# Optimization experiments

Hardware: AMD Instinct MI355X
Metric: run time of the kernel (lower is better)

## Reference

```python
import jax, jax.numpy as jnp
import numpy as np

G, N, F, H, B, L = 4, 1024, 256, 256, 32, 4


def setup_inputs() -> dict:
    key = jax.random.key(0)
    ks = jax.random.split(key, 8)
    batch_xs = jax.random.normal(ks[0], (G, N, F), dtype=jnp.float32)
    # dense (preprocessed/normalized) adjacency; scale ~1/N keeps activations stable
    batch_as = jax.random.uniform(ks[1], (G, N, N), dtype=jnp.float32) / N
    w_in = jax.random.normal(ks[2], (F, H), dtype=jnp.float32) * 0.05
    b_in = jnp.zeros((H,), dtype=jnp.float32)
    gcn_w = jax.random.normal(ks[3], (L, H, H), dtype=jnp.float32) * 0.05
    gcn_b = jnp.zeros((L, H), dtype=jnp.float32)
    graph_idx = jax.random.randint(ks[4], (B,), 0, G)
    cp_mask = jax.random.randint(ks[5], (B, N), 0, 2).astype(bool)
    return {"batch_xs": batch_xs, "batch_as": batch_as, "w_in": w_in, "b_in": b_in,
            "gcn_w": gcn_w, "gcn_b": gcn_b, "graph_idx": graph_idx, "cp_mask": cp_mask}


def reference(batch_xs, batch_as, w_in, b_in, gcn_w, gcn_b, graph_idx, cp_mask):
    # gather_nd: select per-example graph features and adjacency
    X = batch_xs[graph_idx]          # [B, N, F]
    A = batch_as[graph_idx]          # [B, N, N]
    # GNN input dense layer (relu); dropout is identity at inference
    x = jax.nn.relu(X @ w_in + b_in)  # [B, N, H]
    res = x                           # residual from post-input activations
    # GCNConv stack: act(A @ x @ W + b); relu for all but final tanh layer
    for i in range(L - 1):
        x = jax.nn.relu(jnp.einsum('bnm,bmh->bnh', A, x) @ gcn_w[i] + gcn_b[i])
    x = jnp.tanh(jnp.einsum('bnm,bmh->bnh', A, x) @ gcn_w[L - 1] + gcn_b[L - 1])
    x = x + res
    # ragged boolean_mask + reduce_mean over nodes == masked mean
    m = cp_mask.astype(x.dtype)       # [B, N]
    denom = jnp.maximum(jnp.sum(m, axis=1, keepdims=True), 1.0)
    return jnp.sum(x * m[..., None], axis=1) / denom  # [B, H]
```

## Files before the change

### kernel.cpp

```cpp
#include <hip/hip_runtime.h>
#include <math.h>

#define G 4
#define NN 1024
#define FF 256
#define HH 256
#define BB 32
#define LL 4

typedef __attribute__((ext_vector_type(8))) short short8;
typedef __attribute__((ext_vector_type(8))) unsigned short ushort8;
typedef __attribute__((ext_vector_type(4))) unsigned short ushort4v;
typedef __attribute__((ext_vector_type(4))) float floatx4;

__device__ inline unsigned short f2bf(float f) {
  union { float f; unsigned u; } x; x.f = f;
  unsigned r = x.u + 0x7fffu + ((x.u >> 16) & 1u);
  return (unsigned short)(r >> 16);
}
__device__ inline float bf2f(unsigned short u) {
  union { unsigned u; float f; } x; x.u = (unsigned)u << 16;
  return x.f;
}

__device__ void in_tile(int job, const float* __restrict__ X,
                        const float* __restrict__ w_in,
                        const float* __restrict__ b_in,
                        unsigned short* __restrict__ xbf,
                        unsigned short* __restrict__ h0bf, unsigned short* As,
                        unsigned short* Bs, int t) {
  const int nt_ = job & 3, mt = (job >> 2) & 15, g = job >> 6;
  const int m0 = mt * 64, n0 = nt_ * 64;
  const int lane = t & 63, w = t >> 6;
  const int wm = w & 1, wn = w >> 1;
  const int l16 = lane & 15, quad = lane >> 4;

  floatx4 acc[2][2];
#pragma unroll
  for (int i = 0; i < 2; ++i)
#pragma unroll
    for (int j = 0; j < 2; ++j) acc[i][j] = (floatx4){0.f, 0.f, 0.f, 0.f};

  for (int tt = 0; tt < 4; ++tt) {
    const int kb = tt * 64;
    __syncthreads();
#pragma unroll
    for (int i = 0; i < 2; ++i) {
      const int q = t + i * 256;
      const int row = q >> 3, c8 = q & 7;
      const float* Af =
          X + (long)g * NN * FF + (long)(m0 + row) * FF + kb + c8 * 8;
      float4 f0 = *(const float4*)Af;
      float4 f1 = *(const float4*)(Af + 4);
      ushort8 v;
      v[0] = f2bf(f0.x); v[1] = f2bf(f0.y); v[2] = f2bf(f0.z); v[3] = f2bf(f0.w);
      v[4] = f2bf(f1.x); v[5] = f2bf(f1.y); v[6] = f2bf(f1.z); v[7] = f2bf(f1.w);
      *(ushort8*)&As[row * 72 + c8 * 8] = v;
    }
    {
      const int row = t >> 2;
      const int c0 = (t & 3) * 16;
#pragma unroll
      for (int j = 0; j < 4; ++j) {
        float4 f = *(const float4*)&w_in[(long)(kb + row) * HH + n0 + c0 + j * 4];
        Bs[(c0 + j * 4 + 0) * 72 + row] = f2bf(f.x);
        Bs[(c0 + j * 4 + 1) * 72 + row] = f2bf(f.y);
        Bs[(c0 + j * 4 + 2) * 72 + row] = f2bf(f.z);
        Bs[(c0 + j * 4 + 3) * 72 + row] = f2bf(f.w);
      }
    }
    __syncthreads();
#pragma unroll
    for (int kk = 0; kk < 64; kk += 32) {
      const int ko = kk + quad * 8;
      short8 a0 = *(const short8*)&As[(wm * 32 + l16) * 72 + ko];
      short8 a1 = *(const short8*)&As[(wm * 32 + 16 + l16) * 72 + ko];
      short8 b0 = *(const short8*)&Bs[(wn * 32 + l16) * 72 + ko];
      short8 b1 = *(const short8*)&Bs[(wn * 32 + 16 + l16) * 72 + ko];
      acc[0][0] = __builtin_amdgcn_mfma_f32_16x16x32_bf16(a0, b0, acc[0][0], 0, 0, 0);
      acc[0][1] = __builtin_amdgcn_mfma_f32_16x16x32_bf16(a0, b1, acc[0][1], 0, 0, 0);
      acc[1][0] = __builtin_amdgcn_mfma_f32_16x16x32_bf16(a1, b0, acc[1][0], 0, 0, 0);
      acc[1][1] = __builtin_amdgcn_mfma_f32_16x16x32_bf16(a1, b1, acc[1][1], 0, 0, 0);
    }
  }

#pragma unroll
  for (int i = 0; i < 2; ++i) {
#pragma unroll
    for (int j = 0; j < 2; ++j) {
      const int n = n0 + wn * 32 + j * 16 + l16;
      const int mB = m0 + wm * 32 + i * 16 + quad * 4;
      const float bv = b_in[n];
#pragma unroll
      for (int r = 0; r < 4; ++r) {
        const unsigned short pv = f2bf(fmaxf(acc[i][j][r] + bv, 0.f));
        xbf[(long)g * NN * HH + (long)(mB + r) * HH + n] = pv;
        h0bf[(long)g * NN * HH + (long)(mB + r) * HH + n] = pv;
      }
    }
  }
}

__device__ void mask_job(int b, const void* __restrict__ cp_mask,
                         float* __restrict__ fmask, float* __restrict__ denom,
                         int t) {
  const unsigned char* bytes = (const unsigned char*)cp_mask;
  __shared__ int fmt;
  __shared__ float red[256];
  if (t == 0) {
    int any = 0;
    for (int i = 0; i < 256; ++i)
      if ((i & 3) && bytes[i]) any = 1;
    fmt = any ? 0 : 1;
  }
  __syncthreads();
  float cnt = 0.f;
  for (int n = t; n < NN; n += 256) {
    float v;
    if (fmt)
      v = ((const int*)cp_mask)[b * NN + n] ? 1.f : 0.f;
    else
      v = bytes[b * NN + n] ? 1.f : 0.f;
    fmask[b * NN + n] = v;
    cnt += v;
  }
  red[t] = cnt;
  __syncthreads();
  for (int s = 128; s > 0; s >>= 1) {
    if (t < s) red[t] += red[t + s];
    __syncthreads();
  }
  if (t == 0) denom[b] = fmaxf(red[0], 1.f);
}

__device__ void gw_job(int j, const float* __restrict__ gcn_w,
                       unsigned short* __restrict__ gwT, int t) {
  const int l = j >> 4, r0 = (j & 15) * 16;
  const float* src = gcn_w + (long)l * HH * HH;
  unsigned short* dst = gwT + (long)l * HH * HH;
  unsigned short vv[16];
#pragma unroll
  for (int rr = 0; rr < 16; ++rr) vv[rr] = f2bf(src[(long)(r0 + rr) * HH + t]);
  *(ushort8*)&dst[(long)t * HH + r0] = *(ushort8*)&vv[0];
  *(ushort8*)&dst[(long)t * HH + r0 + 8] = *(ushort8*)&vv[8];
}

__global__ __launch_bounds__(256) void pre_kernel(
    const float* __restrict__ batch_as, unsigned short* __restrict__ Abf,
    const float* __restrict__ batch_xs, const float* __restrict__ w_in,
    const float* __restrict__ b_in, unsigned short* __restrict__ xbf,
    unsigned short* __restrict__ h0bf, const float* __restrict__ gcn_w,
    unsigned short* __restrict__ gwT, const void* __restrict__ cp_mask,
    float* __restrict__ fmask, float* __restrict__ denom,
    float* __restrict__ out) {
  __shared__ __align__(16) unsigned short As[64 * 72];
  __shared__ __align__(16) unsigned short Bs[64 * 72];
  const int b = blockIdx.x, t = threadIdx.x;
  if (b < 1024) {
    const long idx = ((long)b * 256 + t) * 16;
#pragma unroll
    for (int h = 0; h < 2; ++h) {
      float4 f0 = *(const float4*)&batch_as[idx + h * 8];
      float4 f1 = *(const float4*)&batch_as[idx + h * 8 + 4];
      ushort8 v;
      v[0] = f2bf(f0.x); v[1] = f2bf(f0.y); v[2] = f2bf(f0.z); v[3] = f2bf(f0.w);
      v[4] = f2bf(f1.x); v[5] = f2bf(f1.y); v[6] = f2bf(f1.z); v[7] = f2bf(f1.w);
      *(ushort8*)&Abf[idx + h * 8] = v;
    }
  } else if (b < 1280) {
    in_tile(b - 1024, batch_xs, w_in, b_in, xbf, h0bf, As, Bs, t);
  } else if (b < 1344) {
    gw_job(b - 1280, gcn_w, gwT, t);
  } else if (b < 1376) {
    mask_job(b - 1344, cp_mask, fmask, denom, t);
  } else {
    for (int i = 0; i < 32; ++i) out[i * 256 + t] = 0.f;
  }
}

__global__ __launch_bounds__(256) void g1_kernel(
    const unsigned short* __restrict__ xbf,
    const unsigned short* __restrict__ WT,
    unsigned short* __restrict__ yT) {
  __shared__ __align__(16) unsigned short As[64 * 72];
  __shared__ __align__(16) unsigned short Bs[64 * 72];
  const int n0 = blockIdx.x * 64;
  const int m0 = blockIdx.y * 64;
  const int g = blockIdx.z;
  const int t = threadIdx.x;
  const int lane = t & 63, w = t >> 6;
  const int wm = w & 1, wn = w >> 1;
  const int l16 = lane & 15, quad = lane >> 4;

  const unsigned short* Ab = xbf + (long)g * NN * HH;

  ushort8 pa[2], pb[2];
  auto load_tile = [&](int tt) {
    const int kb = tt * 64;
#pragma unroll
    for (int i = 0; i < 2; ++i) {
      const int q = t + i * 256;
      const int row = q >> 3, c8 = q & 7;
      pa[i] = *(const ushort8*)&Ab[(long)(m0 + row) * HH + kb + c8 * 8];
      pb[i] = *(const ushort8*)&WT[(long)(n0 + row) * HH + kb + c8 * 8];
    }
  };
  auto store_tile = [&]() {
#pragma unroll
    for (int i = 0; i < 2; ++i) {
      const int q = t + i * 256;
      const int row = q >> 3, c8 = q & 7;
      *(ushort8*)&As[row * 72 + c8 * 8] = pa[i];
      *(ushort8*)&Bs[row * 72 + c8 * 8] = pb[i];
    }
  };

  floatx4 acc[2][2];
#pragma unroll
  for (int i = 0; i < 2; ++i)
#pragma unroll
    for (int j = 0; j < 2; ++j) acc[i][j] = (floatx4){0.f, 0.f, 0.f, 0.f};

  load_tile(0);
  for (int tt = 0; tt < 4; ++tt) {
    __syncthreads();
    store_tile();
    __syncthreads();
    if (tt + 1 < 4) load_tile(tt + 1);
#pragma unroll
    for (int kk = 0; kk < 64; kk += 32) {
      const int ko = kk + quad * 8;
      short8 a0 = *(const short8*)&As[(wm * 32 + l16) * 72 + ko];
      short8 a1 = *(const short8*)&As[(wm * 32 + 16 + l16) * 72 + ko];
      short8 b0 = *(const short8*)&Bs[(wn * 32 + l16) * 72 + ko];
      short8 b1 = *(const short8*)&Bs[(wn * 32 + 16 + l16) * 72 + ko];
      acc[0][0] = __builtin_amdgcn_mfma_f32_16x16x32_bf16(a0, b0, acc[0][0], 0, 0, 0);
      acc[0][1] = __builtin_amdgcn_mfma_f32_16x16x32_bf16(a0, b1, acc[0][1], 0, 0, 0);
      acc[1][0] = __builtin_amdgcn_mfma_f32_16x16x32_bf16(a1, b0, acc[1][0], 0, 0, 0);
      acc[1][1] = __builtin_amdgcn_mfma_f32_16x16x32_bf16(a1, b1, acc[1][1], 0, 0, 0);
    }
  }

#pragma unroll
  for (int i = 0; i < 2; ++i) {
#pragma unroll
    for (int j = 0; j < 2; ++j) {
      const int n = n0 + wn * 32 + j * 16 + l16;
      const int mB = m0 + wm * 32 + i * 16 + quad * 4;
      ushort4v pv;
#pragma unroll
      for (int r = 0; r < 4; ++r) pv[r] = f2bf(acc[i][j][r]);
      *(ushort4v*)&yT[(long)g * HH * NN + (long)n * NN + mB] = pv;
    }
  }
}

template <int ACT>
__global__ __launch_bounds__(256) void g2_kernel(
    const unsigned short* __restrict__ Abf,
    const unsigned short* __restrict__ yT, const float* __restrict__ bias,
    const unsigned short* __restrict__ h0bf, unsigned short* __restrict__ xbf,
    const float* __restrict__ fmask, const float* __restrict__ denom,
    const int* __restrict__ gidx, float* __restrict__ out) {
  __shared__ __align__(16) unsigned short As[32 * 136];
  __shared__ __align__(16) unsigned short Bs[64 * 136];
  const int n0 = blockIdx.x * 64;
  const int m0 = blockIdx.y * 32;
  const int g = blockIdx.z;
  const int t = threadIdx.x;
  const int lane = t & 63, w = t >> 6;
  const int wm = w & 1, wn = w >> 1;
  const int l16 = lane & 15, quad = lane >> 4;

  const unsigned short* Ag = Abf + (long)g * NN * NN + (long)m0 * NN;
  const unsigned short* Bg = yT + (long)g * HH * NN + (long)n0 * NN;

  ushort8 pa[2], pb[4];
  auto load_tile = [&](int tt) {
    const int kb = tt * 128;
#pragma unroll
    for (int i = 0; i < 2; ++i) {
      const int q = t + i * 256;
      const int row = q >> 4, c8 = q & 15;
      pa[i] = *(const ushort8*)&Ag[(long)row * NN + kb + c8 * 8];
    }
#pragma unroll
    for (int i = 0; i < 4; ++i) {
      const int q = t + i * 256;
      const int row = q >> 4, c8 = q & 15;
      pb[i] = *(const ushort8*)&Bg[(long)row * NN + kb + c8 * 8];
    }
  };
  auto store_tile = [&]() {
#pragma unroll
    for (int i = 0; i < 2; ++i) {
      const int q = t + i * 256;
      const int row = q >> 4, c8 = q & 15;
      *(ushort8*)&As[row * 136 + c8 * 8] = pa[i];
    }
#pragma unroll
    for (int i = 0; i < 4; ++i) {
      const int q = t + i * 256;
      const int row = q >> 4, c8 = q & 15;
      *(ushort8*)&Bs[row * 136 + c8 * 8] = pb[i];
    }
  };

  floatx4 acc[2];
  acc[0] = (floatx4){0.f, 0.f, 0.f, 0.f};
  acc[1] = (floatx4){0.f, 0.f, 0.f, 0.f};

  load_tile(0);
  for (int tt = 0; tt < 8; ++tt) {
    __syncthreads();
    store_tile();
    __syncthreads();
    if (tt + 1 < 8) load_tile(tt + 1);
#pragma unroll
    for (int kk = 0; kk < 128; kk += 32) {
      const int ko = kk + quad * 8;
      short8 a = *(const short8*)&As[(wm * 16 + l16) * 136 + ko];
      short8 b0 = *(const short8*)&Bs[(wn * 32 + l16) * 136 + ko];
      short8 b1 = *(const short8*)&Bs[(wn * 32 + 16 + l16) * 136 + ko];
      acc[0] = __builtin_amdgcn_mfma_f32_16x16x32_bf16(a, b0, acc[0], 0, 0, 0);
      acc[1] = __builtin_amdgcn_mfma_f32_16x16x32_bf16(a, b1, acc[1], 0, 0, 0);
    }
  }

  if (ACT == 1) {
#pragma unroll
    for (int j = 0; j < 2; ++j) {
      const int n = n0 + wn * 32 + j * 16 + l16;
      const int mB = m0 + wm * 16 + quad * 4;
      const float bv = bias[n];
#pragma unroll
      for (int r = 0; r < 4; ++r)
        xbf[(long)g * NN * HH + (long)(mB + r) * HH + n] =
            f2bf(fmaxf(acc[j][r] + bv, 0.f));
    }
  } else {
    const int mB0 = m0 + wm * 16 + quad * 4;
    float zv[2][4];
#pragma unroll
    for (int j = 0; j < 2; ++j) {
      const int n = n0 + wn * 32 + j * 16 + l16;
      const float bv = bias[n];
#pragma unroll
      for (int r = 0; r < 4; ++r) {
        const long idx = (long)g * NN * HH + (long)(mB0 + r) * HH + n;
        zv[j][r] = tanhf(acc[j][r] + bv) + bf2f(h0bf[idx]);
      }
    }
    for (int b = 0; b < BB; ++b) {
      if (gidx[b] != g) continue;
      const float invd = 1.f / denom[b];
      float m4[4];
#pragma unroll
      for (int r = 0; r < 4; ++r) m4[r] = fmask[b * NN + mB0 + r];
#pragma unroll
      for (int j = 0; j < 2; ++j) {
        float p = m4[0] * zv[j][0] + m4[1] * zv[j][1] + m4[2] * zv[j][2] +
                  m4[3] * zv[j][3];
        p += __shfl_xor(p, 16);
        p += __shfl_xor(p, 32);
        if (quad == 0) {
          const int n = n0 + wn * 32 + j * 16 + l16;
          atomicAdd(&out[b * HH + n], p * invd);
        }
      }
    }
  }
}

extern "C" void kernel_launch(void* const* d_in, const int* in_sizes, int n_in,
                              void* d_out, int out_size, void* d_ws,
                              size_t ws_size, hipStream_t stream) {
  (void)in_sizes; (void)n_in; (void)out_size; (void)ws_size;
  const float* batch_xs = (const float*)d_in[0];
  const float* batch_as = (const float*)d_in[1];
  const float* w_in = (const float*)d_in[2];
  const float* b_in = (const float*)d_in[3];
  const float* gcn_w = (const float*)d_in[4];
  const float* gcn_b = (const float*)d_in[5];
  const int* graph_idx = (const int*)d_in[6];
  const void* cp_mask = d_in[7];
  float* out = (float*)d_out;

  char* p = (char*)d_ws;
  unsigned short* Abf = (unsigned short*)p;  p += (long)G * NN * NN * 2;
  unsigned short* gwT = (unsigned short*)p;  p += (long)LL * HH * HH * 2;
  unsigned short* xbf = (unsigned short*)p;  p += (long)G * NN * HH * 2;
  unsigned short* h0bf = (unsigned short*)p; p += (long)G * NN * HH * 2;
  unsigned short* yT = (unsigned short*)p;   p += (long)G * HH * NN * 2;
  float* fmask = (float*)p;                  p += (long)BB * NN * 4;
  float* denom = (float*)p;                  p += BB * 4;

  pre_kernel<<<1377, 256, 0, stream>>>(batch_as, Abf, batch_xs, w_in, b_in,
                                       xbf, h0bf, gcn_w, gwT, cp_mask, fmask,
                                       denom, out);

  for (int l = 0; l < LL; ++l) {
    g1_kernel<<<dim3(4, 16, G), 256, 0, stream>>>(
        xbf, gwT + (long)l * HH * HH, yT);
    if (l < LL - 1)
      g2_kernel<1><<<dim3(4, 32, G), 256, 0, stream>>>(
          Abf, yT, gcn_b + (long)l * HH, nullptr, xbf, nullptr, nullptr,
          nullptr, nullptr);
    else
      g2_kernel<0><<<dim3(4, 32, G), 256, 0, stream>>>(
          Abf, yT, gcn_b + (long)l * HH, h0bf, nullptr, fmask, denom,
          graph_idx, out);
  }
}
```

Measured before the change: 147.1 us.

## Fuse adjacency matmul with next layer's weight matmul per row block

Adds a fused kernel that computes relu(A@y + b) for a 16-row block and immediately multiplies it by the next layer's weight matrix, writing the transposed result directly. This replaces the separate g1/g2 launch pairs for the middle layers, removing the intermediate xbf round-trip and three kernel launches. In exchange the grid is much smaller (256 blocks of 512 threads) with a large shared-memory footprint, and each block re-reads the full transposed y for its graph, which may lower occupancy and parallelism.

```diff
diff --git a/kernel.cpp b/kernel.cpp
--- a/kernel.cpp
+++ b/kernel.cpp
@@ -252,6 +252,127 @@
       for (int r = 0; r < 4; ++r) pv[r] = f2bf(acc[i][j][r]);
       *(ushort4v*)&yT[(long)g * HH * NN + (long)n * NN + mB] = pv;
     }
+  }
+}
+
+__global__ __launch_bounds__(512) void fused_kernel(
+    const unsigned short* __restrict__ Abf,
+    const unsigned short* __restrict__ yT, const float* __restrict__ bias,
+    const unsigned short* __restrict__ WT, unsigned short* __restrict__ y2T) {
+  __shared__ __align__(16) unsigned short As[16 * 136];
+  __shared__ __align__(16) unsigned short Bs[256 * 136];
+  __shared__ __align__(16) unsigned short Xs[16 * 264];
+  const int m0 = blockIdx.x * 16;
+  const int g = blockIdx.y;
+  const int t = threadIdx.x;
+  const int lane = t & 63, w = t >> 6;
+  const int l16 = lane & 15, quad = lane >> 4;
+
+  const unsigned short* Ag = Abf + (long)g * NN * NN + (long)m0 * NN;
+  const unsigned short* Bg = yT + (long)g * HH * NN;
+
+  ushort8 pb[8], pa;
+  auto load_tile = [&](int tt) {
+    const int kb = tt * 128;
+#pragma unroll
+    for (int i = 0; i < 8; ++i) {
+      const int q = t + i * 512;
+      const int row = q >> 4, c8 = q & 15;
+      pb[i] = *(const ushort8*)&Bg[(long)row * NN + kb + c8 * 8];
+    }
+    if (t < 256) {
+      const int row = t >> 4, c8 = t & 15;
+      pa = *(const ushort8*)&Ag[(long)row * NN + kb + c8 * 8];
+    }
+  };
+  auto store_tile = [&]() {
+#pragma unroll
+    for (int i = 0; i < 8; ++i) {
+      const int q = t + i * 512;
+      const int row = q >> 4, c8 = q & 15;
+      *(ushort8*)&Bs[row * 136 + c8 * 8] = pb[i];
+    }
+    if (t < 256) {
+      const int row = t >> 4, c8 = t & 15;
+      *(ushort8*)&As[row * 136 + c8 * 8] = pa;
+    }
+  };
+
+  floatx4 acc[2];
+  acc[0] = (floatx4){0.f, 0.f, 0.f, 0.f};
+  acc[1] = (floatx4){0.f, 0.f, 0.f, 0.f};
+
+  load_tile(0);
+  for (int tt = 0; tt < 8; ++tt) {
+    __syncthreads();
+    store_tile();
+    __syncthreads();
+    if (tt + 1 < 8) load_tile(tt + 1);
+#pragma unroll
+    for (int kk = 0; kk < 128; kk += 32) {
+      const int ko = kk + quad * 8;
+      short8 a = *(const short8*)&As[l16 * 136 + ko];
+      short8 b0 = *(const short8*)&Bs[(w * 32 + l16) * 136 + ko];
+      short8 b1 = *(const short8*)&Bs[(w * 32 + 16 + l16) * 136 + ko];
+      acc[0] = __builtin_amdgcn_mfma_f32_16x16x32_bf16(a, b0, acc[0], 0, 0, 0);
+      acc[1] = __builtin_amdgcn_mfma_f32_16x16x32_bf16(a, b1, acc[1], 0, 0, 0);
+    }
+  }
+
+  ushort8 pw[8];
+  auto loadW = [&](int t2) {
+    const int kb = t2 * 128;
+#pragma unroll
+    for (int i = 0; i < 8; ++i) {
+      const int q = t + i * 512;
+      const int row = q >> 4, c8 = q & 15;
+      pw[i] = *(const ushort8*)&WT[(long)row * HH + kb + c8 * 8];
+    }
+  };
+  loadW(0);
+
+#pragma unroll
+  for (int j = 0; j < 2; ++j) {
+    const int n = w * 32 + j * 16 + l16;
+    const float bv = bias[n];
+#pragma unroll
+    for (int r = 0; r < 4; ++r)
+      Xs[(quad * 4 + r) * 264 + n] = f2bf(fmaxf(acc[j][r] + bv, 0.f));
+  }
+
+  floatx4 acc2[2];
+  acc2[0] = (floatx4){0.f, 0.f, 0.f, 0.f};
+  acc2[1] = (floatx4){0.f, 0.f, 0.f, 0.f};
+
+  for (int t2 = 0; t2 < 2; ++t2) {
+    __syncthreads();
+#pragma unroll
+    for (int i = 0; i < 8; ++i) {
+      const int q = t + i * 512;
+      const int row = q >> 4, c8 = q & 15;
+      *(ushort8*)&Bs[row * 136 + c8 * 8] = pw[i];
+    }
+    __syncthreads();
+    if (t2 == 0) loadW(1);
+    const int kb = t2 * 128;
+#pragma unroll
+    for (int kk = 0; kk < 128; kk += 32) {
+      const int ko = kk + quad * 8;
+      short8 a = *(const short8*)&Xs[l16 * 264 + kb + ko];
+      short8 b0 = *(const short8*)&Bs[(w * 32 + l16) * 136 + ko];
+      short8 b1 = *(const short8*)&Bs[(w * 32 + 16 + l16) * 136 + ko];
+      acc2[0] = __builtin_amdgcn_mfma_f32_16x16x32_bf16(a, b0, acc2[0], 0, 0, 0);
+      acc2[1] = __builtin_amdgcn_mfma_f32_16x16x32_bf16(a, b1, acc2[1], 0, 0, 0);
+    }
+  }
+
+#pragma unroll
+  for (int j = 0; j < 2; ++j) {
+    const int n = w * 32 + j * 16 + l16;
+    ushort4v pv;
+#pragma unroll
+    for (int r = 0; r < 4; ++r) pv[r] = f2bf(acc2[j][r]);
+    *(ushort4v*)&y2T[(long)g * HH * NN + (long)n * NN + m0 + quad * 4] = pv;
   }
 }
 
@@ -391,7 +512,8 @@
   unsigned short* gwT = (unsigned short*)p;  p += (long)LL * HH * HH * 2;
   unsigned short* xbf = (unsigned short*)p;  p += (long)G * NN * HH * 2;
   unsigned short* h0bf = (unsigned short*)p; p += (long)G * NN * HH * 2;
-  unsigned short* yT = (unsigned short*)p;   p += (long)G * HH * NN * 2;
+  unsigned short* yTa = (unsigned short*)p;  p += (long)G * HH * NN * 2;
+  unsigned short* yTb = (unsigned short*)p;  p += (long)G * HH * NN * 2;
   float* fmask = (float*)p;                  p += (long)BB * NN * 4;
   float* denom = (float*)p;                  p += BB * 4;
 
@@ -399,16 +521,16 @@
                                        xbf, h0bf, gcn_w, gwT, cp_mask, fmask,
                                        denom, out);
 
-  for (int l = 0; l < LL; ++l) {
-    g1_kernel<<<dim3(4, 16, G), 256, 0, stream>>>(
-        xbf, gwT + (long)l * HH * HH, yT);
-    if (l < LL - 1)
-      g2_kernel<1><<<dim3(4, 32, G), 256, 0, stream>>>(
-          Abf, yT, gcn_b + (long)l * HH, nullptr, xbf, nullptr, nullptr,
-          nullptr, nullptr);
-    else
-      g2_kernel<0><<<dim3(4, 32, G), 256, 0, stream>>>(
-          Abf, yT, gcn_b + (long)l * HH, h0bf, nullptr, fmask, denom,
-          graph_idx, out);
-  }
-}
+  g1_kernel<<<dim3(4, 16, G), 256, 0, stream>>>(xbf, gwT, yTa);
+
+  fused_kernel<<<dim3(64, G), 512, 0, stream>>>(
+      Abf, yTa, gcn_b + 0 * HH, gwT + (long)1 * HH * HH, yTb);
+  fused_kernel<<<dim3(64, G), 512, 0, stream>>>(
+      Abf, yTb, gcn_b + 1 * HH, gwT + (long)2 * HH * HH, yTa);
+  fused_kernel<<<dim3(64, G), 512, 0, stream>>>(
+      Abf, yTa, gcn_b + 2 * HH, gwT + (long)3 * HH * HH, yTb);
+
+  g2_kernel<0><<<dim3(4, 32, G), 256, 0, stream>>>(
+      Abf, yTb, gcn_b + (long)3 * HH, h0bf, nullptr, fmask, denom,
+      graph_idx, out);
+}
```

Measured after the change: 149.5 us. About the same (+1.7%).

## Fuse input layer with first GCN weight matmul in pre-kernel

Applied to the files above, without the earlier changes.

The pre-kernel's input dense-layer tiles now compute full 64x256 row blocks and chain straight into the layer-0 weight matmul, writing the transposed product directly. This removes the first g1_kernel launch and the xbf round trip for layer 0, and ping-pongs between two yT buffers. The cost is far fewer, heavier tiles (64 blocks instead of 256) that use much more shared memory and registers, and the output zeroing is folded into the mask blocks.

```diff
diff --git a/kernel.cpp b/kernel.cpp
--- a/kernel.cpp
+++ b/kernel.cpp
@@ -23,23 +23,21 @@
   return x.f;
 }
 
-__device__ void in_tile(int job, const float* __restrict__ X,
-                        const float* __restrict__ w_in,
-                        const float* __restrict__ b_in,
-                        unsigned short* __restrict__ xbf,
-                        unsigned short* __restrict__ h0bf, unsigned short* As,
-                        unsigned short* Bs, int t) {
-  const int nt_ = job & 3, mt = (job >> 2) & 15, g = job >> 6;
-  const int m0 = mt * 64, n0 = nt_ * 64;
+__device__ void in64_tile(int job, const float* __restrict__ X,
+                          const float* __restrict__ w_in,
+                          const float* __restrict__ b_in,
+                          const float* __restrict__ gcn_w0,
+                          unsigned short* __restrict__ h0bf,
+                          unsigned short* __restrict__ yT, unsigned short* As,
+                          unsigned short* Bs, unsigned short* Xs, int t) {
+  const int mt = job & 15, g = job >> 4;
+  const int m0 = mt * 64;
   const int lane = t & 63, w = t >> 6;
-  const int wm = w & 1, wn = w >> 1;
   const int l16 = lane & 15, quad = lane >> 4;
 
-  floatx4 acc[2][2];
-#pragma unroll
-  for (int i = 0; i < 2; ++i)
-#pragma unroll
-    for (int j = 0; j < 2; ++j) acc[i][j] = (floatx4){0.f, 0.f, 0.f, 0.f};
+  floatx4 acc[16];
+#pragma unroll
+  for (int j = 0; j < 16; ++j) acc[j] = (floatx4){0.f, 0.f, 0.f, 0.f};
 
   for (int tt = 0; tt < 4; ++tt) {
     const int kb = tt * 64;
@@ -61,43 +59,88 @@
       const int row = t >> 2;
       const int c0 = (t & 3) * 16;
 #pragma unroll
-      for (int j = 0; j < 4; ++j) {
-        float4 f = *(const float4*)&w_in[(long)(kb + row) * HH + n0 + c0 + j * 4];
-        Bs[(c0 + j * 4 + 0) * 72 + row] = f2bf(f.x);
-        Bs[(c0 + j * 4 + 1) * 72 + row] = f2bf(f.y);
-        Bs[(c0 + j * 4 + 2) * 72 + row] = f2bf(f.z);
-        Bs[(c0 + j * 4 + 3) * 72 + row] = f2bf(f.w);
+      for (int nb = 0; nb < 4; ++nb) {
+#pragma unroll
+        for (int jj = 0; jj < 4; ++jj) {
+          float4 f = *(const float4*)&w_in[(long)(kb + row) * HH + nb * 64 +
+                                           c0 + jj * 4];
+          Bs[(nb * 64 + c0 + jj * 4 + 0) * 72 + row] = f2bf(f.x);
+          Bs[(nb * 64 + c0 + jj * 4 + 1) * 72 + row] = f2bf(f.y);
+          Bs[(nb * 64 + c0 + jj * 4 + 2) * 72 + row] = f2bf(f.z);
+          Bs[(nb * 64 + c0 + jj * 4 + 3) * 72 + row] = f2bf(f.w);
+        }
       }
     }
     __syncthreads();
 #pragma unroll
     for (int kk = 0; kk < 64; kk += 32) {
       const int ko = kk + quad * 8;
-      short8 a0 = *(const short8*)&As[(wm * 32 + l16) * 72 + ko];
-      short8 a1 = *(const short8*)&As[(wm * 32 + 16 + l16) * 72 + ko];
-      short8 b0 = *(const short8*)&Bs[(wn * 32 + l16) * 72 + ko];
-      short8 b1 = *(const short8*)&Bs[(wn * 32 + 16 + l16) * 72 + ko];
-      acc[0][0] = __builtin_amdgcn_mfma_f32_16x16x32_bf16(a0, b0, acc[0][0], 0, 0, 0);
-      acc[0][1] = __builtin_amdgcn_mfma_f32_16x16x32_bf16(a0, b1, acc[0][1], 0, 0, 0);
-      acc[1][0] = __builtin_amdgcn_mfma_f32_16x16x32_bf16(a1, b0, acc[1][0], 0, 0, 0);
-      acc[1][1] = __builtin_amdgcn_mfma_f32_16x16x32_bf16(a1, b1, acc[1][1], 0, 0, 0);
-    }
-  }
-
-#pragma unroll
-  for (int i = 0; i < 2; ++i) {
-#pragma unroll
-    for (int j = 0; j < 2; ++j) {
-      const int n = n0 + wn * 32 + j * 16 + l16;
-      const int mB = m0 + wm * 32 + i * 16 + quad * 4;
-      const float bv = b_in[n];
-#pragma unroll
-      for (int r = 0; r < 4; ++r) {
-        const unsigned short pv = f2bf(fmaxf(acc[i][j][r] + bv, 0.f));
-        xbf[(long)g * NN * HH + (long)(mB + r) * HH + n] = pv;
-        h0bf[(long)g * NN * HH + (long)(mB + r) * HH + n] = pv;
-      }
-    }
+      short8 a = *(const short8*)&As[(w * 16 + l16) * 72 + ko];
+#pragma unroll
+      for (int j = 0; j < 16; ++j) {
+        short8 b = *(const short8*)&Bs[(j * 16 + l16) * 72 + ko];
+        acc[j] = __builtin_amdgcn_mfma_f32_16x16x32_bf16(a, b, acc[j], 0, 0, 0);
+      }
+    }
+  }
+
+#pragma unroll
+  for (int j = 0; j < 16; ++j) {
+    const int n = j * 16 + l16;
+    const float bv = b_in[n];
+#pragma unroll
+    for (int r = 0; r < 4; ++r) {
+      const int mr = w * 16 + quad * 4 + r;
+      const unsigned short pv = f2bf(fmaxf(acc[j][r] + bv, 0.f));
+      h0bf[(long)g * NN * HH + (long)(m0 + mr) * HH + n] = pv;
+      Xs[mr * 264 + n] = pv;
+    }
+  }
+
+  floatx4 acc2[16];
+#pragma unroll
+  for (int j = 0; j < 16; ++j) acc2[j] = (floatx4){0.f, 0.f, 0.f, 0.f};
+
+  for (int tt = 0; tt < 4; ++tt) {
+    const int kb = tt * 64;
+    __syncthreads();
+    {
+      const int row = t >> 2;
+      const int c0 = (t & 3) * 16;
+#pragma unroll
+      for (int nb = 0; nb < 4; ++nb) {
+#pragma unroll
+        for (int jj = 0; jj < 4; ++jj) {
+          float4 f = *(const float4*)&gcn_w0[(long)(kb + row) * HH + nb * 64 +
+                                             c0 + jj * 4];
+          Bs[(nb * 64 + c0 + jj * 4 + 0) * 72 + row] = f2bf(f.x);
+          Bs[(nb * 64 + c0 + jj * 4 + 1) * 72 + row] = f2bf(f.y);
+          Bs[(nb * 64 + c0 + jj * 4 + 2) * 72 + row] = f2bf(f.z);
+          Bs[(nb * 64 + c0 + jj * 4 + 3) * 72 + row] = f2bf(f.w);
+        }
+      }
+    }
+    __syncthreads();
+#pragma unroll
+    for (int kk = 0; kk < 64; kk += 32) {
+      const int ko = kk + quad * 8;
+      short8 a = *(const short8*)&Xs[(w * 16 + l16) * 264 + kb + ko];
+#pragma unroll
+      for (int j = 0; j < 16; ++j) {
+        short8 b = *(const short8*)&Bs[(j * 16 + l16) * 72 + ko];
+        acc2[j] = __builtin_amdgcn_mfma_f32_16x16x32_bf16(a, b, acc2[j], 0, 0, 0);
+      }
+    }
+  }
+
+#pragma unroll
+  for (int j = 0; j < 16; ++j) {
+    const int n = j * 16 + l16;
+    ushort4v pv;
+#pragma unroll
+    for (int r = 0; r < 4; ++r) pv[r] = f2bf(acc2[j][r]);
+    *(ushort4v*)&yT[(long)g * HH * NN + (long)n * NN + m0 + w * 16 + quad * 4] =
+        pv;
   }
 }
 
@@ -145,16 +188,17 @@
   *(ushort8*)&dst[(long)t * HH + r0 + 8] = *(ushort8*)&vv[8];
 }
 
-__global__ __launch_bounds__(256) void pre_kernel(
+__global__ __launch_bounds__(256) void pre64_kernel(
     const float* __restrict__ batch_as, unsigned short* __restrict__ Abf,
     const float* __restrict__ batch_xs, const float* __restrict__ w_in,
-    const float* __restrict__ b_in, unsigned short* __restrict__ xbf,
-    unsigned short* __restrict__ h0bf, const float* __restrict__ gcn_w,
+    const float* __restrict__ b_in, const float* __restrict__ gcn_w,
+    unsigned short* __restrict__ h0bf, unsigned short* __restrict__ yT0,
     unsigned short* __restrict__ gwT, const void* __restrict__ cp_mask,
     float* __restrict__ fmask, float* __restrict__ denom,
     float* __restrict__ out) {
   __shared__ __align__(16) unsigned short As[64 * 72];
-  __shared__ __align__(16) unsigned short Bs[64 * 72];
+  __shared__ __align__(16) unsigned short Bs[256 * 72];
+  __shared__ __align__(16) unsigned short Xs[64 * 264];
   const int b = blockIdx.x, t = threadIdx.x;
   if (b < 1024) {
     const long idx = ((long)b * 256 + t) * 16;
@@ -167,14 +211,14 @@
       v[4] = f2bf(f1.x); v[5] = f2bf(f1.y); v[6] = f2bf(f1.z); v[7] = f2bf(f1.w);
       *(ushort8*)&Abf[idx + h * 8] = v;
     }
-  } else if (b < 1280) {
-    in_tile(b - 1024, batch_xs, w_in, b_in, xbf, h0bf, As, Bs, t);
-  } else if (b < 1344) {
-    gw_job(b - 1280, gcn_w, gwT, t);
-  } else if (b < 1376) {
-    mask_job(b - 1344, cp_mask, fmask, denom, t);
+  } else if (b < 1088) {
+    in64_tile(b - 1024, batch_xs, w_in, b_in, gcn_w, h0bf, yT0, As, Bs, Xs, t);
+  } else if (b < 1136) {
+    gw_job(16 + (b - 1088), gcn_w, gwT, t);
   } else {
-    for (int i = 0; i < 32; ++i) out[i * 256 + t] = 0.f;
+    const int bb = b - 1136;
+    out[bb * HH + t] = 0.f;
+    mask_job(bb, cp_mask, fmask, denom, t);
   }
 }
 
@@ -391,24 +435,31 @@
   unsigned short* gwT = (unsigned short*)p;  p += (long)LL * HH * HH * 2;
   unsigned short* xbf = (unsigned short*)p;  p += (long)G * NN * HH * 2;
   unsigned short* h0bf = (unsigned short*)p; p += (long)G * NN * HH * 2;
-  unsigned short* yT = (unsigned short*)p;   p += (long)G * HH * NN * 2;
+  unsigned short* yTa = (unsigned short*)p;  p += (long)G * HH * NN * 2;
+  unsigned short* yTb = (unsigned short*)p;  p += (long)G * HH * NN * 2;
   float* fmask = (float*)p;                  p += (long)BB * NN * 4;
   float* denom = (float*)p;                  p += BB * 4;
 
-  pre_kernel<<<1377, 256, 0, stream>>>(batch_as, Abf, batch_xs, w_in, b_in,
-                                       xbf, h0bf, gcn_w, gwT, cp_mask, fmask,
-                                       denom, out);
-
-  for (int l = 0; l < LL; ++l) {
-    g1_kernel<<<dim3(4, 16, G), 256, 0, stream>>>(
-        xbf, gwT + (long)l * HH * HH, yT);
-    if (l < LL - 1)
-      g2_kernel<1><<<dim3(4, 32, G), 256, 0, stream>>>(
-          Abf, yT, gcn_b + (long)l * HH, nullptr, xbf, nullptr, nullptr,
-          nullptr, nullptr);
-    else
-      g2_kernel<0><<<dim3(4, 32, G), 256, 0, stream>>>(
-          Abf, yT, gcn_b + (long)l * HH, h0bf, nullptr, fmask, denom,
-          graph_idx, out);
-  }
-}
+  pre64_kernel<<<1168, 256, 0, stream>>>(batch_as, Abf, batch_xs, w_in, b_in,
+                                         gcn_w, h0bf, yTa, gwT, cp_mask,
+                                         fmask, denom, out);
+
+  g2_kernel<1><<<dim3(4, 32, G), 256, 0, stream>>>(
+      Abf, yTa, gcn_b + 0 * HH, nullptr, xbf, nullptr, nullptr, nullptr,
+      nullptr);
+  g1_kernel<<<dim3(4, 16, G), 256, 0, stream>>>(xbf, gwT + (long)1 * HH * HH,
+                                                yTb);
+  g2_kernel<1><<<dim3(4, 32, G), 256, 0, stream>>>(
+      Abf, yTb, gcn_b + 1 * HH, nullptr, xbf, nullptr, nullptr, nullptr,
+      nullptr);
+  g1_kernel<<<dim3(4, 16, G), 256, 0, stream>>>(xbf, gwT + (long)2 * HH * HH,
+                                                yTa);
+  g2_kernel<1><<<dim3(4, 32, G), 256, 0, stream>>>(
+      Abf, yTa, gcn_b + 2 * HH, nullptr, xbf, nullptr, nullptr, nullptr,
+      nullptr);
+  g1_kernel<<<dim3(4, 16, G), 256, 0, stream>>>(xbf, gwT + (long)3 * HH * HH,
+                                                yTb);
+  g2_kernel<0><<<dim3(4, 32, G), 256, 0, stream>>>(
+      Abf, yTb, gcn_b + (long)3 * HH, h0bf, nullptr, fmask, denom, graph_idx,
+      out);
+}
```

After: 163.8 us. 1.11x slower.

## Drop LDS staging in GEMM kernels and read MFMA fragments directly from global

Applied to the files above, without the earlier changes.

Both the feature-transform GEMM and the adjacency GEMM now load MFMA operand fragments straight from global memory into registers, dropping the shared-memory tiles and the two barriers per k-step. The intent is to cut LDS traffic and synchronisation stalls and to rely on L1/L2 caching for operand reuse across waves. The y buffer is double-buffered and the launch order is restructured so the next layer's g1 writes into the alternate buffer. The risk is more global/L2 traffic and exposed latency, since there is no longer any software prefetch and each wave re-reads shared operands.

```diff
diff --git a/kernel.cpp b/kernel.cpp
--- a/kernel.cpp
+++ b/kernel.cpp
@@ -178,12 +178,10 @@
   }
 }
 
-__global__ __launch_bounds__(256) void g1_kernel(
+__global__ __launch_bounds__(256) void g1_nolds(
     const unsigned short* __restrict__ xbf,
     const unsigned short* __restrict__ WT,
     unsigned short* __restrict__ yT) {
-  __shared__ __align__(16) unsigned short As[64 * 72];
-  __shared__ __align__(16) unsigned short Bs[64 * 72];
   const int n0 = blockIdx.x * 64;
   const int m0 = blockIdx.y * 64;
   const int g = blockIdx.z;
@@ -192,28 +190,11 @@
   const int wm = w & 1, wn = w >> 1;
   const int l16 = lane & 15, quad = lane >> 4;
 
-  const unsigned short* Ab = xbf + (long)g * NN * HH;
-
-  ushort8 pa[2], pb[2];
-  auto load_tile = [&](int tt) {
-    const int kb = tt * 64;
-#pragma unroll
-    for (int i = 0; i < 2; ++i) {
-      const int q = t + i * 256;
-      const int row = q >> 3, c8 = q & 7;
-      pa[i] = *(const ushort8*)&Ab[(long)(m0 + row) * HH + kb + c8 * 8];
-      pb[i] = *(const ushort8*)&WT[(long)(n0 + row) * HH + kb + c8 * 8];
-    }
-  };
-  auto store_tile = [&]() {
-#pragma unroll
-    for (int i = 0; i < 2; ++i) {
-      const int q = t + i * 256;
-      const int row = q >> 3, c8 = q & 7;
-      *(ushort8*)&As[row * 72 + c8 * 8] = pa[i];
-      *(ushort8*)&Bs[row * 72 + c8 * 8] = pb[i];
-    }
-  };
+  const unsigned short* Ar0 =
+      xbf + (long)g * NN * HH + (long)(m0 + wm * 32 + l16) * HH + quad * 8;
+  const unsigned short* Ar1 = Ar0 + 16 * HH;
+  const unsigned short* Br0 = WT + (long)(n0 + wn * 32 + l16) * HH + quad * 8;
+  const unsigned short* Br1 = Br0 + 16 * HH;
 
   floatx4 acc[2][2];
 #pragma unroll
@@ -221,24 +202,16 @@
 #pragma unroll
     for (int j = 0; j < 2; ++j) acc[i][j] = (floatx4){0.f, 0.f, 0.f, 0.f};
 
-  load_tile(0);
-  for (int tt = 0; tt < 4; ++tt) {
-    __syncthreads();
-    store_tile();
-    __syncthreads();
-    if (tt + 1 < 4) load_tile(tt + 1);
-#pragma unroll
-    for (int kk = 0; kk < 64; kk += 32) {
-      const int ko = kk + quad * 8;
-      short8 a0 = *(const short8*)&As[(wm * 32 + l16) * 72 + ko];
-      short8 a1 = *(const short8*)&As[(wm * 32 + 16 + l16) * 72 + ko];
-      short8 b0 = *(const short8*)&Bs[(wn * 32 + l16) * 72 + ko];
-      short8 b1 = *(const short8*)&Bs[(wn * 32 + 16 + l16) * 72 + ko];
-      acc[0][0] = __builtin_amdgcn_mfma_f32_16x16x32_bf16(a0, b0, acc[0][0], 0, 0, 0);
-      acc[0][1] = __builtin_amdgcn_mfma_f32_16x16x32_bf16(a0, b1, acc[0][1], 0, 0, 0);
-      acc[1][0] = __builtin_amdgcn_mfma_f32_16x16x32_bf16(a1, b0, acc[1][0], 0, 0, 0);
-      acc[1][1] = __builtin_amdgcn_mfma_f32_16x16x32_bf16(a1, b1, acc[1][1], 0, 0, 0);
-    }
+#pragma unroll
+  for (int kk = 0; kk < HH; kk += 32) {
+    short8 a0 = *(const short8*)(Ar0 + kk);
+    short8 a1 = *(const short8*)(Ar1 + kk);
+    short8 b0 = *(const short8*)(Br0 + kk);
+    short8 b1 = *(const short8*)(Br1 + kk);
+    acc[0][0] = __builtin_amdgcn_mfma_f32_16x16x32_bf16(a0, b0, acc[0][0], 0, 0, 0);
+    acc[0][1] = __builtin_amdgcn_mfma_f32_16x16x32_bf16(a0, b1, acc[0][1], 0, 0, 0);
+    acc[1][0] = __builtin_amdgcn_mfma_f32_16x16x32_bf16(a1, b0, acc[1][0], 0, 0, 0);
+    acc[1][1] = __builtin_amdgcn_mfma_f32_16x16x32_bf16(a1, b1, acc[1][1], 0, 0, 0);
   }
 
 #pragma unroll
@@ -256,14 +229,12 @@
 }
 
 template <int ACT>
-__global__ __launch_bounds__(256) void g2_kernel(
+__global__ __launch_bounds__(256) void g2_nolds(
     const unsigned short* __restrict__ Abf,
     const unsigned short* __restrict__ yT, const float* __restrict__ bias,
     const unsigned short* __restrict__ h0bf, unsigned short* __restrict__ xbf,
     const float* __restrict__ fmask, const float* __restrict__ denom,
     const int* __restrict__ gidx, float* __restrict__ out) {
-  __shared__ __align__(16) unsigned short As[32 * 136];
-  __shared__ __align__(16) unsigned short Bs[64 * 136];
   const int n0 = blockIdx.x * 64;
   const int m0 = blockIdx.y * 32;
   const int g = blockIdx.z;
@@ -272,59 +243,23 @@
   const int wm = w & 1, wn = w >> 1;
   const int l16 = lane & 15, quad = lane >> 4;
 
-  const unsigned short* Ag = Abf + (long)g * NN * NN + (long)m0 * NN;
-  const unsigned short* Bg = yT + (long)g * HH * NN + (long)n0 * NN;
-
-  ushort8 pa[2], pb[4];
-  auto load_tile = [&](int tt) {
-    const int kb = tt * 128;
-#pragma unroll
-    for (int i = 0; i < 2; ++i) {
-      const int q = t + i * 256;
-      const int row = q >> 4, c8 = q & 15;
-      pa[i] = *(const ushort8*)&Ag[(long)row * NN + kb + c8 * 8];
-    }
-#pragma unroll
-    for (int i = 0; i < 4; ++i) {
-      const int q = t + i * 256;
-      const int row = q >> 4, c8 = q & 15;
-      pb[i] = *(const ushort8*)&Bg[(long)row * NN + kb + c8 * 8];
-    }
-  };
-  auto store_tile = [&]() {
-#pragma unroll
-    for (int i = 0; i < 2; ++i) {
-      const int q = t + i * 256;
-      const int row = q >> 4, c8 = q & 15;
-      *(ushort8*)&As[row * 136 + c8 * 8] = pa[i];
-    }
-#pragma unroll
-    for (int i = 0; i < 4; ++i) {
-      const int q = t + i * 256;
-      const int row = q >> 4, c8 = q & 15;
-      *(ushort8*)&Bs[row * 136 + c8 * 8] = pb[i];
-    }
-  };
+  const unsigned short* Ar =
+      Abf + (long)g * NN * NN + (long)(m0 + wm * 16 + l16) * NN + quad * 8;
+  const unsigned short* Br0 =
+      yT + (long)g * HH * NN + (long)(n0 + wn * 32 + l16) * NN + quad * 8;
+  const unsigned short* Br1 = Br0 + 16 * NN;
 
   floatx4 acc[2];
   acc[0] = (floatx4){0.f, 0.f, 0.f, 0.f};
   acc[1] = (floatx4){0.f, 0.f, 0.f, 0.f};
 
-  load_tile(0);
-  for (int tt = 0; tt < 8; ++tt) {
-    __syncthreads();
-    store_tile();
-    __syncthreads();
-    if (tt + 1 < 8) load_tile(tt + 1);
-#pragma unroll
-    for (int kk = 0; kk < 128; kk += 32) {
-      const int ko = kk + quad * 8;
-      short8 a = *(const short8*)&As[(wm * 16 + l16) * 136 + ko];
-      short8 b0 = *(const short8*)&Bs[(wn * 32 + l16) * 136 + ko];
-      short8 b1 = *(const short8*)&Bs[(wn * 32 + 16 + l16) * 136 + ko];
-      acc[0] = __builtin_amdgcn_mfma_f32_16x16x32_bf16(a, b0, acc[0], 0, 0, 0);
-      acc[1] = __builtin_amdgcn_mfma_f32_16x16x32_bf16(a, b1, acc[1], 0, 0, 0);
-    }
+#pragma unroll 4
+  for (int kk = 0; kk < NN; kk += 32) {
+    short8 a = *(const short8*)(Ar + kk);
+    short8 b0 = *(const short8*)(Br0 + kk);
+    short8 b1 = *(const short8*)(Br1 + kk);
+    acc[0] = __builtin_amdgcn_mfma_f32_16x16x32_bf16(a, b0, acc[0], 0, 0, 0);
+    acc[1] = __builtin_amdgcn_mfma_f32_16x16x32_bf16(a, b1, acc[1], 0, 0, 0);
   }
 
   if (ACT == 1) {
@@ -391,7 +326,8 @@
   unsigned short* gwT = (unsigned short*)p;  p += (long)LL * HH * HH * 2;
   unsigned short* xbf = (unsigned short*)p;  p += (long)G * NN * HH * 2;
   unsigned short* h0bf = (unsigned short*)p; p += (long)G * NN * HH * 2;
-  unsigned short* yT = (unsigned short*)p;   p += (long)G * HH * NN * 2;
+  unsigned short* yTa = (unsigned short*)p;  p += (long)G * HH * NN * 2;
+  unsigned short* yTb = (unsigned short*)p;  p += (long)G * HH * NN * 2;
   float* fmask = (float*)p;                  p += (long)BB * NN * 4;
   float* denom = (float*)p;                  p += BB * 4;
 
@@ -399,16 +335,21 @@
                                        xbf, h0bf, gcn_w, gwT, cp_mask, fmask,
                                        denom, out);
 
+  g1_nolds<<<dim3(4, 16, G), 256, 0, stream>>>(xbf, gwT, yTa);
+
   for (int l = 0; l < LL; ++l) {
-    g1_kernel<<<dim3(4, 16, G), 256, 0, stream>>>(
-        xbf, gwT + (long)l * HH * HH, yT);
-    if (l < LL - 1)
-      g2_kernel<1><<<dim3(4, 32, G), 256, 0, stream>>>(
-          Abf, yT, gcn_b + (long)l * HH, nullptr, xbf, nullptr, nullptr,
+    const unsigned short* ycur = (l & 1) ? yTb : yTa;
+    unsigned short* ynext = (l & 1) ? yTa : yTb;
+    if (l < LL - 1) {
+      g2_nolds<1><<<dim3(4, 32, G), 256, 0, stream>>>(
+          Abf, ycur, gcn_b + (long)l * HH, nullptr, xbf, nullptr, nullptr,
           nullptr, nullptr);
-    else
-      g2_kernel<0><<<dim3(4, 32, G), 256, 0, stream>>>(
-          Abf, yT, gcn_b + (long)l * HH, h0bf, nullptr, fmask, denom,
+      g1_nolds<<<dim3(4, 16, G), 256, 0, stream>>>(
+          xbf, gwT + (long)(l + 1) * HH * HH, ynext);
+    } else {
+      g2_nolds<0><<<dim3(4, 32, G), 256, 0, stream>>>(
+          Abf, ycur, gcn_b + (long)l * HH, h0bf, nullptr, fmask, denom,
           graph_idx, out);
-  }
-}
+    }
+  }
+}
```

Result: slower. 211.8 us (+44.0%).
